# Optimization experiments

Hardware: AMD Instinct MI355X
Metric: run time of the kernel (lower is better)

Reference implementation:

```python
import jax, jax.numpy as jnp
import numpy as np

N_EMBD = 2048
N_HEAD = 16
N_INNER = 8192
EPS = 1e-5


def _wn_weight(v, g):
    # torch weight_norm with dim=1 on weight [out, in]:
    # w[:, j] = g[j] * v[:, j] / ||v[:, j]||_2
    norm = jnp.sqrt(jnp.sum(v * v, axis=0))  # [in]
    return v * (g / norm)[None, :]


def _layer_norm(x, gamma, beta):
    mu = jnp.mean(x, axis=-1, keepdims=True)
    var = jnp.mean(jnp.square(x - mu), axis=-1, keepdims=True)
    return (x - mu) * jax.lax.rsqrt(var + EPS) * gamma + beta


def setup_inputs() -> dict:
    key = jax.random.key(0)
    ks = jax.random.split(key, 12)
    E, I, H = N_EMBD, N_INNER, N_HEAD
    s = lambda n: 1.0 / np.sqrt(n)
    return {
        "hidden_states": jax.random.normal(ks[0], (2, 2048, E), jnp.float32),
        "ln1_g": jnp.ones((E,), jnp.float32),
        "ln1_b": jnp.zeros((E,), jnp.float32),
        "w_qkv": jax.random.normal(ks[1], (3 * E, E), jnp.float32) * s(E),
        "b_qkv": jnp.zeros((3 * E,), jnp.float32),
        "attn_proj_v": jax.random.normal(ks[2], (E, E), jnp.float32) * s(E),
        "attn_proj_g": jnp.abs(jax.random.normal(ks[3], (E,), jnp.float32)) + 0.5,
        "attn_proj_b": jnp.zeros((E,), jnp.float32),
        "emotion_bias": jax.random.normal(ks[4], (H,), jnp.float32) * 0.1,
        "ln2_g": jnp.ones((E,), jnp.float32),
        "ln2_b": jnp.zeros((E,), jnp.float32),
        "w_fc": jax.random.normal(ks[5], (I, E), jnp.float32) * s(E),
        "b_fc": jnp.zeros((I,), jnp.float32),
        "mlp_proj_v": jax.random.normal(ks[6], (E, I), jnp.float32) * s(I),
        "mlp_proj_g": jnp.abs(jax.random.normal(ks[7], (I,), jnp.float32)) + 0.5,
        "mlp_proj_b": jnp.zeros((E,), jnp.float32),
    }


def reference(hidden_states, ln1_g, ln1_b, w_qkv, b_qkv, attn_proj_v, attn_proj_g,
              attn_proj_b, emotion_bias, ln2_g, ln2_b, w_fc, b_fc,
              mlp_proj_v, mlp_proj_g, mlp_proj_b):
    B, S, E = hidden_states.shape
    H = N_HEAD
    D = E // H

    # --- attention sub-block ---
    residual = hidden_states
    x = _layer_norm(hidden_states, ln1_g, ln1_b)
    qkv = x @ w_qkv.T + b_qkv                       # [B,S,3E]
    q, k, v = jnp.split(qkv, 3, axis=-1)
    q = q.reshape(B, S, H, D).transpose(0, 2, 1, 3)  # [B,H,S,D]
    k = k.reshape(B, S, H, D).transpose(0, 2, 1, 3)
    v = v.reshape(B, S, H, D).transpose(0, 2, 1, 3)

    scores = jnp.einsum("bhqd,bhkd->bhqk", q, k) / jnp.sqrt(jnp.float32(D))
    scores = scores + emotion_bias[None, :, None, None]
    probs = jax.nn.softmax(scores, axis=-1)
    attn = jnp.einsum("bhqk,bhkd->bhqd", probs, v)   # [B,H,S,D]
    attn = attn.transpose(0, 2, 1, 3).reshape(B, S, E)
    w_proj = _wn_weight(attn_proj_v, attn_proj_g)
    attn = attn @ w_proj.T + attn_proj_b

    hidden = attn + residual

    # --- MLP sub-block ---
    residual = hidden
    x = _layer_norm(hidden, ln2_g, ln2_b)
    h = jax.nn.gelu(x @ w_fc.T + b_fc, approximate=False)
    w_proj2 = _wn_weight(mlp_proj_v, mlp_proj_g)
    h = h @ w_proj2.T + mlp_proj_b
    return residual + h
```

## Files before the change

### kernel.cpp

```cpp
#include <hip/hip_runtime.h>
#include <hip/hip_bf16.h>

#define DEVI __device__ __forceinline__

typedef __attribute__((ext_vector_type(8))) __bf16 bf16x8;
typedef __attribute__((ext_vector_type(4))) float f32x4;
typedef __attribute__((ext_vector_type(4))) unsigned short u16x4;
typedef __attribute__((ext_vector_type(8))) unsigned short u16x8;

DEVI unsigned short f2bf(float f) {
  unsigned int u = __float_as_uint(f);
  u += 0x7FFFu + ((u >> 16) & 1u);
  return (unsigned short)(u >> 16);
}

#define GLD16(g, l) __builtin_amdgcn_global_load_lds(                      \
    (const __attribute__((address_space(1))) void*)(g),                    \
    (__attribute__((address_space(3))) void*)(l), 16, 0, 0)


__global__ __launch_bounds__(256) void cast_k(const float* __restrict__ in,
                                              unsigned short* __restrict__ out,
                                              int n4) {
  for (int i = blockIdx.x * 256 + threadIdx.x; i < n4; i += gridDim.x * 256) {
    f32x4 v = ((const f32x4*)in)[i];
    u16x4 o;
    o.x = f2bf(v.x); o.y = f2bf(v.y); o.z = f2bf(v.z); o.w = f2bf(v.w);
    ((u16x4*)out)[i] = o;
  }
}

__global__ __launch_bounds__(256) void colnorm1_k(const float* __restrict__ v,
                                                  float* __restrict__ part,
                                                  int cols) {
  const int tid = threadIdx.x;
  const int g = tid & 127;
  const int s = tid >> 7;
  const int c0 = blockIdx.x * 512;
  const int r0 = blockIdx.y * 64 + s * 32;
  const float* base = v + (size_t)r0 * cols + c0 + g * 4;
  f32x4 acc = {};
#pragma unroll 4
  for (int i = 0; i < 32; ++i) {
    f32x4 x = *(const f32x4*)(base + (size_t)i * cols);
    acc.x += x.x * x.x; acc.y += x.y * x.y;
    acc.z += x.z * x.z; acc.w += x.w * x.w;
  }
  __shared__ f32x4 red[256];
  red[tid] = acc;
  __syncthreads();
  if (s == 0) {
    f32x4 a = red[tid], b = red[tid + 128];
    f32x4 o;
    o.x = a.x + b.x; o.y = a.y + b.y; o.z = a.z + b.z; o.w = a.w + b.w;
    *(f32x4*)(part + (size_t)blockIdx.y * cols + c0 + g * 4) = o;
  }
}

__global__ __launch_bounds__(256) void colnorm2_k(const float* __restrict__ part,
                                                  const float* __restrict__ g,
                                                  float* __restrict__ s,
                                                  int cols, int nrc) {
  const int c = blockIdx.x * 256 + threadIdx.x;
  float acc = 0.f;
  for (int i = 0; i < nrc; ++i) acc += part[(size_t)i * cols + c];
  s[c] = g[c] * rsqrtf(acc);
}

__global__ __launch_bounds__(256) void scale_cast_k(const float* __restrict__ in,
                                                    const float* __restrict__ s,
                                                    unsigned short* __restrict__ out,
                                                    int cols, int n4) {
  const int cmask4 = (cols >> 2) - 1;
  for (int i = blockIdx.x * 256 + threadIdx.x; i < n4; i += gridDim.x * 256) {
    f32x4 v = ((const f32x4*)in)[i];
    f32x4 sv = ((const f32x4*)s)[i & cmask4];
    u16x4 o;
    o.x = f2bf(v.x * sv.x); o.y = f2bf(v.y * sv.y);
    o.z = f2bf(v.z * sv.z); o.w = f2bf(v.w * sv.w);
    ((u16x4*)out)[i] = o;
  }
}

__global__ __launch_bounds__(256) void ln_k(const float* __restrict__ x,
                                            const float* __restrict__ g,
                                            const float* __restrict__ b,
                                            unsigned short* __restrict__ out) {
  const int tid = threadIdx.x, lane = tid & 63, wid = tid >> 6;
  const int row = blockIdx.x;
  const float* xr = x + (size_t)row * 2048;
  f32x4 a0 = ((const f32x4*)xr)[tid];
  f32x4 a1 = ((const f32x4*)xr)[tid + 256];
  float s = a0.x + a0.y + a0.z + a0.w + a1.x + a1.y + a1.z + a1.w;
  float ss = a0.x * a0.x + a0.y * a0.y + a0.z * a0.z + a0.w * a0.w +
             a1.x * a1.x + a1.y * a1.y + a1.z * a1.z + a1.w * a1.w;
#pragma unroll
  for (int m = 1; m < 64; m <<= 1) {
    s += __shfl_xor(s, m);
    ss += __shfl_xor(ss, m);
  }
  __shared__ float red[8];
  if (lane == 0) { red[wid] = s; red[4 + wid] = ss; }
  __syncthreads();
  s = red[0] + red[1] + red[2] + red[3];
  ss = red[4] + red[5] + red[6] + red[7];
  const float mu = s * (1.f / 2048.f);
  const float var = ss * (1.f / 2048.f) - mu * mu;
  const float rs = rsqrtf(var + 1e-5f);
  f32x4 g0 = ((const f32x4*)g)[tid], g1 = ((const f32x4*)g)[tid + 256];
  f32x4 b0 = ((const f32x4*)b)[tid], b1 = ((const f32x4*)b)[tid + 256];
  u16x4 o0, o1;
  o0.x = f2bf((a0.x - mu) * rs * g0.x + b0.x);
  o0.y = f2bf((a0.y - mu) * rs * g0.y + b0.y);
  o0.z = f2bf((a0.z - mu) * rs * g0.z + b0.z);
  o0.w = f2bf((a0.w - mu) * rs * g0.w + b0.w);
  o1.x = f2bf((a1.x - mu) * rs * g1.x + b1.x);
  o1.y = f2bf((a1.y - mu) * rs * g1.y + b1.y);
  o1.z = f2bf((a1.z - mu) * rs * g1.z + b1.z);
  o1.w = f2bf((a1.w - mu) * rs * g1.w + b1.w);
  unsigned short* orow = out + (size_t)row * 2048;
  *(u16x4*)(orow + 4 * tid) = o0;
  *(u16x4*)(orow + 1024 + 4 * tid) = o1;
}

__global__ __launch_bounds__(256) void vtrans_k(const unsigned short* __restrict__ v,
                                                unsigned short* __restrict__ vt) {
  __shared__ unsigned short t[64][134];
  const int tid = threadIdx.x;
  const int bh = blockIdx.x >> 5, st = blockIdx.x & 31;
  const unsigned short* vb = v + ((size_t)bh << 18) + ((size_t)(st << 6) << 7);
#pragma unroll
  for (int i = 0; i < 4; ++i) {
    int f = tid + (i << 8);
    int row = f >> 4, c8 = f & 15;
    u16x8 x = *(const u16x8*)(vb + row * 128 + c8 * 8);
#pragma unroll
    for (int j = 0; j < 4; ++j) {
      unsigned int pk = ((unsigned int)x[2 * j + 1] << 16) | x[2 * j];
      *(unsigned int*)&t[row][c8 * 8 + 2 * j] = pk;
    }
  }
  __syncthreads();
  const int lane = tid & 63, wid = tid >> 6;
  unsigned short* ob = vt + ((size_t)bh << 18) + (st << 6);
#pragma unroll
  for (int j = 0; j < 32; ++j) {
    int d = (wid << 5) + j;
    ob[((size_t)d << 11) + lane] = t[lane][d];
  }
}

__global__ __launch_bounds__(256) void g4red_k(const float* __restrict__ p0,
                                               const float* __restrict__ p1,
                                               const float* __restrict__ bias,
                                               const float* __restrict__ res,
                                               float* __restrict__ out, int n4) {
  for (int i = blockIdx.x * 256 + threadIdx.x; i < n4; i += gridDim.x * 256) {
    f32x4 a = ((const f32x4*)p0)[i];
    f32x4 b = ((const f32x4*)p1)[i];
    f32x4 r = ((const f32x4*)res)[i];
    f32x4 bb = ((const f32x4*)bias)[i & 511];
    f32x4 o;
    o.x = a.x + b.x + r.x + bb.x;
    o.y = a.y + b.y + r.y + bb.y;
    o.z = a.z + b.z + r.z + bb.z;
    o.w = a.w + b.w + r.w + bb.w;
    ((f32x4*)out)[i] = o;
  }
}

struct GemmP {
  const unsigned short* A;
  const unsigned short* B;
  const float* bias;
  const float* res;
  float* outF;
  unsigned short* outH;
  unsigned short* q;
  unsigned short* k;
  unsigned short* vt;
  int M, N, K;
};

template <int EPI>
DEVI void gemm128_body(const GemmP& p, int m0, int n0, int k0, int nk) {
  const int tid = threadIdx.x, lane = tid & 63, wid = tid >> 6;
  const int K = p.K;
  const int wr = wid >> 1, wc = wid & 1;

  __shared__ __align__(16) unsigned short sA[2][4096];
  __shared__ __align__(16) unsigned short sB[2][4096];

  const int c0 = tid, c1 = tid + 256;
  const unsigned short* gA0 = p.A + (size_t)(m0 + (c0 >> 2)) * K + k0 + ((c0 & 3) << 3);
  const unsigned short* gA1 = p.A + (size_t)(m0 + (c1 >> 2)) * K + k0 + ((c1 & 3) << 3);
  const unsigned short* gB0 = p.B + (size_t)(n0 + (c0 >> 2)) * K + k0 + ((c0 & 3) << 3);
  const unsigned short* gB1 = p.B + (size_t)(n0 + (c1 >> 2)) * K + k0 + ((c1 & 3) << 3);
  const int l0 = wid << 9, l1 = (wid << 9) + 2048;

  f32x4 acc[4][4] = {};
  const int arow = (wr << 6) + (lane & 15);
  const int brow = (wc << 6) + (lane & 15);
  const int koff = (lane >> 4) << 3;

#define STAGE128(bufi, t) do { int ko = (t) << 5;       \
    GLD16(gA0 + ko, &sA[bufi][l0]);                     \
    GLD16(gA1 + ko, &sA[bufi][l1]);                     \
    GLD16(gB0 + ko, &sB[bufi][l0]);                     \
    GLD16(gB1 + ko, &sB[bufi][l1]); } while (0)

  STAGE128(0, 0);
  __syncthreads();
  int cur = 0;
  for (int t = 0; t < nk; ++t) {
    if (t + 1 < nk) STAGE128(cur ^ 1, t + 1);
    bf16x8 af[4], bfr[4];
#pragma unroll
    for (int i = 0; i < 4; ++i)
      af[i] = *(const bf16x8*)&sA[cur][(arow + (i << 4)) * 32 + koff];
#pragma unroll
    for (int i = 0; i < 4; ++i)
      bfr[i] = *(const bf16x8*)&sB[cur][(brow + (i << 4)) * 32 + koff];
#pragma unroll
    for (int i = 0; i < 4; ++i)
#pragma unroll
      for (int j = 0; j < 4; ++j)
        acc[i][j] = __builtin_amdgcn_mfma_f32_16x16x32_bf16(af[i], bfr[j], acc[i][j], 0, 0, 0);
    __syncthreads();
    cur ^= 1;
  }
#undef STAGE128

  const int rbase = m0 + (wr << 6) + ((lane >> 4) << 2);
  const int cbase = n0 + (wc << 6) + (lane & 15);
#pragma unroll
  for (int mi = 0; mi < 4; ++mi) {
#pragma unroll
    for (int ni = 0; ni < 4; ++ni) {
      const int col = cbase + (ni << 4);
#pragma unroll
      for (int r = 0; r < 4; ++r) {
        const int row = rbase + (mi << 4) + r;
        if constexpr (EPI == 0) {
          float v = acc[mi][ni][r] + p.bias[col];
          const int gsel = col >> 11, e = col & 2047;
          const int h = e >> 7, d = e & 127;
          const int b2 = row >> 11, sidx = row & 2047;
          const size_t off = ((size_t)(b2 * 16 + h) << 18) + ((size_t)sidx << 7) + d;
          unsigned short hv = f2bf(v);
          if (gsel == 0)      p.q[off] = hv;
          else if (gsel == 1) p.k[off] = hv;
          else                p.vt[off] = hv;
        } else if constexpr (EPI == 1) {
          const size_t o = (size_t)row * p.N + col;
          p.outF[o] = acc[mi][ni][r] + p.bias[col] + p.res[o];
        } else {
          p.outF[(size_t)row * p.N + col] = acc[mi][ni][r];
        }
      }
    }
  }
}

__global__ __launch_bounds__(256) void g1_qkv128(GemmP p) {
  const int x = blockIdx.x & 7, i = blockIdx.x >> 3;
  const int bm = i & 31;
  const int bn = x * 6 + (i >> 5);
  gemm128_body<0>(p, bm << 7, bn << 7, 0, p.K >> 5);
}
__global__ __launch_bounds__(256) void g2_proj128(GemmP p) {
  const int x = blockIdx.x & 7, i = blockIdx.x >> 3;
  const int bm = (x >> 1) * 8 + (i >> 3);
  const int bn = (x & 1) * 8 + (i & 7);
  gemm128_body<1>(p, bm << 7, bn << 7, 0, p.K >> 5);
}
__global__ __launch_bounds__(256) void g4_splitk(GemmP p) {
  const int x = blockIdx.x & 7, i = blockIdx.x >> 3;
  const int ks = i & 1, j = i >> 1;
  const int bm = (x >> 1) * 8 + (j >> 3);
  const int bn = (x & 1) * 8 + (j & 7);
  GemmP q = p;
  q.outF = p.outF + (size_t)ks * 4096 * 2048;
  gemm128_body<4>(q, bm << 7, bn << 7, ks << 12, 128);
}

DEVI void setup256(const GemmP& p, int m0, int n0,
                   const unsigned short*& gsA0, const unsigned short*& gsA1,
                   const unsigned short*& gsB0, const unsigned short*& gsB1) {
  const int tid = threadIdx.x;
  int r_[2], c_[2];
#pragma unroll
  for (int j = 0; j < 2; ++j) {
    int d = tid * 16 + j * 8192;
    int w = (d & 1023) ^ (((d >> 9) & 1) << 5);
    r_[j] = ((d >> 10) << 4) + (w >> 6);
    c_[j] = (w & 63) >> 1;
  }
  gsA0 = p.A + (size_t)(m0 + r_[0]) * p.K + c_[0];
  gsA1 = p.A + (size_t)(m0 + r_[1]) * p.K + c_[1];
  gsB0 = p.B + (size_t)(n0 + r_[0]) * p.K + c_[0];
  gsB1 = p.B + (size_t)(n0 + r_[1]) * p.K + c_[1];
}

DEVI void epi256g(const GemmP& p, f32x4 (&acc)[8][4], int m0, int n0) {
  const int lane = threadIdx.x & 63, wid = threadIdx.x >> 6;
  const int wr = wid >> 2, wc = wid & 3;
  const int lr = lane & 15, lk = lane >> 4;
  const int rbase = m0 + wr * 128 + (lk << 2);
  const int cbase = n0 + wc * 64 + lr;
#pragma unroll
  for (int m = 0; m < 8; ++m) {
#pragma unroll
    for (int n = 0; n < 4; ++n) {
      const int col = cbase + (n << 4);
      const float bb = p.bias[col];
#pragma unroll
      for (int r = 0; r < 4; ++r) {
        const int row = rbase + (m << 4) + r;
        float v = acc[m][n][r] + bb;
        float y = 0.7978845608028654f * (v + 0.044715f * v * v * v);
        float u = __expf(2.f * y);
        float gl = (y > 40.f) ? v : v * (u / (u + 1.f));
        p.outH[(size_t)row * p.N + col] = f2bf(gl);
      }
    }
  }
}

DEVI void gemm8p_body(const GemmP& p, unsigned short* lds_raw, int m0, int n0) {
  const int tid = threadIdx.x, lane = tid & 63, wid = tid >> 6;
  const int wr = wid >> 2, wc = wid & 3;
  const int lr = lane & 15, lk = lane >> 4;
  const int fb = (lr * 64 + lk * 16) ^ ((lr & 8) << 2);

  const unsigned short *gsA0, *gsA1, *gsB0, *gsB1;
  setup256(p, m0, n0, gsA0, gsA1, gsB0, gsB1);

#define STAGE_A8(b, kt) do { unsigned short* _d = lds_raw + ((b) << 14);       \
    GLD16(gsA0 + ((size_t)(kt) << 5), _d + (tid << 3));                        \
    GLD16(gsA1 + ((size_t)(kt) << 5), _d + 4096 + (tid << 3)); } while (0)
#define STAGE_B8(b, kt) do { unsigned short* _d = lds_raw + ((b) << 14) + 8192;\
    GLD16(gsB0 + ((size_t)(kt) << 5), _d + (tid << 3));                        \
    GLD16(gsB1 + ((size_t)(kt) << 5), _d + 4096 + (tid << 3)); } while (0)

  f32x4 acc[8][4] = {};
  const int NK = p.K >> 5;

  STAGE_A8(0, 0); STAGE_B8(0, 0);
  STAGE_A8(1, 1); STAGE_B8(1, 1);
  STAGE_A8(2, 2); STAGE_B8(2, 2);
  asm volatile("s_waitcnt vmcnt(8)" ::: "memory");
  __builtin_amdgcn_s_barrier();

  for (int t = 0; t < NK; ++t) {
    const int bi = t & 3;
    const char* tA = (const char*)(lds_raw + (bi << 14));
    const char* tB = (const char*)(lds_raw + (bi << 14) + 8192);
    bf16x8 a_[4], b_[4];
#pragma unroll
    for (int n = 0; n < 4; ++n)
      b_[n] = *(const bf16x8*)(tB + (((wc << 2) + n) << 10) + fb);
#pragma unroll
    for (int m = 0; m < 4; ++m)
      a_[m] = *(const bf16x8*)(tA + (((wr << 3) + m) << 10) + fb);
    if (t + 3 < NK) STAGE_A8((t + 3) & 3, t + 3);
    __builtin_amdgcn_s_barrier();
    asm volatile("s_waitcnt lgkmcnt(0)" ::: "memory");
    __builtin_amdgcn_sched_barrier(0);
    __builtin_amdgcn_s_setprio(1);
#pragma unroll
    for (int m = 0; m < 4; ++m)
#pragma unroll
      for (int n = 0; n < 4; ++n)
        acc[m][n] = __builtin_amdgcn_mfma_f32_16x16x32_bf16(a_[m], b_[n], acc[m][n], 0, 0, 0);
    __builtin_amdgcn_s_setprio(0);
    __builtin_amdgcn_s_barrier();
#pragma unroll
    for (int m = 0; m < 4; ++m)
      a_[m] = *(const bf16x8*)(tA + (((wr << 3) + 4 + m) << 10) + fb);
    if (t + 3 < NK) STAGE_B8((t + 3) & 3, t + 3);
    if (t + 3 < NK)      asm volatile("s_waitcnt vmcnt(8)" ::: "memory");
    else if (t + 2 < NK) asm volatile("s_waitcnt vmcnt(4)" ::: "memory");
    else if (t + 1 < NK) asm volatile("s_waitcnt vmcnt(0)" ::: "memory");
    __builtin_amdgcn_s_barrier();
    asm volatile("s_waitcnt lgkmcnt(0)" ::: "memory");
    __builtin_amdgcn_sched_barrier(0);
    __builtin_amdgcn_s_setprio(1);
#pragma unroll
    for (int m = 0; m < 4; ++m)
#pragma unroll
      for (int n = 0; n < 4; ++n)
        acc[4 + m][n] = __builtin_amdgcn_mfma_f32_16x16x32_bf16(a_[m], b_[n], acc[4 + m][n], 0, 0, 0);
    __builtin_amdgcn_s_setprio(0);
    __builtin_amdgcn_s_barrier();
  }
#undef STAGE_A8
#undef STAGE_B8
  epi256g(p, acc, m0, n0);
}

DEVI void gemm2p_body(const GemmP& p, unsigned short* lds_raw, int m0, int n0) {
  const int tid = threadIdx.x, lane = tid & 63, wid = tid >> 6;
  const int wr = wid >> 2, wc = wid & 3;
  const int lr = lane & 15, lk = lane >> 4;
  const int fb = (lr * 64 + lk * 16) ^ ((lr & 8) << 2);

  const unsigned short *gsA0, *gsA1, *gsB0, *gsB1;
  setup256(p, m0, n0, gsA0, gsA1, gsB0, gsB1);

#define STG2(b, kt) do { unsigned short* _d = lds_raw + ((b) << 14);     \
    GLD16(gsA0 + ((size_t)(kt) << 5), _d + (tid << 3));                  \
    GLD16(gsA1 + ((size_t)(kt) << 5), _d + 4096 + (tid << 3));           \
    GLD16(gsB0 + ((size_t)(kt) << 5), _d + 8192 + (tid << 3));           \
    GLD16(gsB1 + ((size_t)(kt) << 5), _d + 12288 + (tid << 3)); } while (0)

  f32x4 acc[8][4] = {};
  const int NK = p.K >> 5;
  STG2(0, 0);
  __syncthreads();
  int cur = 0;
  for (int t = 0; t < NK; ++t) {
    if (t + 1 < NK) STG2(cur ^ 1, t + 1);
    const char* tA = (const char*)(lds_raw + (cur << 14));
    const char* tB = tA + 16384;
    bf16x8 a_[8], b_[4];
#pragma unroll
    for (int n = 0; n < 4; ++n)
      b_[n] = *(const bf16x8*)(tB + (((wc << 2) + n) << 10) + fb);
#pragma unroll
    for (int m = 0; m < 8; ++m)
      a_[m] = *(const bf16x8*)(tA + (((wr << 3) + m) << 10) + fb);
#pragma unroll
    for (int m = 0; m < 8; ++m)
#pragma unroll
      for (int n = 0; n < 4; ++n)
        acc[m][n] = __builtin_amdgcn_mfma_f32_16x16x32_bf16(a_[m], b_[n], acc[m][n], 0, 0, 0);
    __syncthreads();
    cur ^= 1;
  }
#undef STG2
  epi256g(p, acc, m0, n0);
}

__global__ __launch_bounds__(512, 2) void g3a_fc8p(GemmP p) {
  extern __shared__ unsigned short lds_raw[];
  const int x = blockIdx.x & 7, i = blockIdx.x >> 3;
  const int bm = (x >> 2) * 4 + (i >> 3);
  const int bn = (x & 3) * 8 + (i & 7);
  gemm8p_body(p, lds_raw, bm << 8, bn << 8);
}
__global__ __launch_bounds__(512, 2) void g3b_fc2p(GemmP p) {
  extern __shared__ unsigned short lds_raw[];
  const int x = blockIdx.x & 7, i = blockIdx.x >> 3;
  const int bm = (x >> 2) * 4 + (i >> 3);
  const int bn = (x & 3) * 8 + (i & 7);
  gemm2p_body(p, lds_raw, 2048 + (bm << 8), bn << 8);
}

__global__ __launch_bounds__(256) void attn_k(const unsigned short* __restrict__ Q,
                                              const unsigned short* __restrict__ Kg,
                                              const unsigned short* __restrict__ Vt,
                                              unsigned short* __restrict__ O) {
  const int tid = threadIdx.x, lane = tid & 63, wid = tid >> 6;
  const int bid = blockIdx.x;
  const int pos = bid >> 3;
  const int bh = (bid & 7) * 4 + (pos >> 5);
  const int qt = pos & 31;
  const int q0 = qt * 64 + wid * 16;
  const int b = bh >> 4, h = bh & 15;

  __shared__ __align__(16) unsigned short sK[64 * 128];
  __shared__ __align__(16) unsigned short sV[128 * 64];
  __shared__ __align__(16) unsigned short sP[4][16 * 72];

  const unsigned short* Qb = Q + ((size_t)bh << 18);
  const unsigned short* Kb = Kg + ((size_t)bh << 18);
  const unsigned short* Vb = Vt + ((size_t)bh << 18);

  bf16x8 qf[4];
  {
    const unsigned short* qp = Qb + (size_t)(q0 + (lane & 15)) * 128 + ((lane >> 4) << 3);
#pragma unroll
    for (int kk = 0; kk < 4; ++kk) qf[kk] = *(const bf16x8*)(qp + kk * 32);
  }

  int koffs[4], voffs[4];
#pragma unroll
  for (int i = 0; i < 4; ++i) {
    const int c = tid + (i << 8);
    const int kv = c >> 4, jj = c & 15;
    const int js = (jj & 8) | ((jj ^ kv) & 7);
    koffs[i] = kv * 128 + (js << 3);
    const int d = c >> 3, j2 = c & 7;
    const int js2 = j2 ^ (d & 7);
    voffs[i] = d * 2048 + (js2 << 3);
  }
  u16x8 kreg[4], vreg[4];
  auto PREF = [&](int kt) {
    const int kv0 = kt << 6;
#pragma unroll
    for (int i = 0; i < 4; ++i) {
      kreg[i] = *(const u16x8*)(Kb + kv0 * 128 + koffs[i]);
      vreg[i] = *(const u16x8*)(Vb + kv0 + voffs[i]);
    }
  };

  f32x4 oacc[8] = {};
  float mrun = -3e38f, lrun = 0.f;
  PREF(0);

  for (int kt = 0; kt < 32; ++kt) {
#pragma unroll
    for (int i = 0; i < 4; ++i) {
      const int c8 = (tid + (i << 8)) << 3;
      *(u16x8*)&sK[c8] = kreg[i];
      *(u16x8*)&sV[c8] = vreg[i];
    }
    __syncthreads();
    if (kt + 1 < 32) PREF(kt + 1);

    f32x4 sc[4] = {};
    __builtin_amdgcn_s_setprio(1);
#pragma unroll
    for (int ti = 0; ti < 4; ++ti) {
#pragma unroll
      for (int kk = 0; kk < 4; ++kk) {
        const int row = (ti << 4) + (lane & 15);
        int bo = (row << 8) + (kk << 6) + ((lane >> 4) << 4);
        bo ^= (row & 7) << 4;
        bf16x8 kf = *(const bf16x8*)((const char*)sK + bo);
        sc[ti] = __builtin_amdgcn_mfma_f32_16x16x32_bf16(kf, qf[kk], sc[ti], 0, 0, 0);
      }
    }
    __builtin_amdgcn_s_setprio(0);

    float pv[16];
    float mx = -3e38f;
#pragma unroll
    for (int ti = 0; ti < 4; ++ti)
#pragma unroll
      for (int r = 0; r < 4; ++r) {
        float x = sc[ti][r] * 0.08838834764831845f;
        pv[(ti << 2) + r] = x;
        mx = fmaxf(mx, x);
      }
    mx = fmaxf(mx, __shfl_xor(mx, 16));
    mx = fmaxf(mx, __shfl_xor(mx, 32));

    float corr = 1.f;
    if (!__all(mx - mrun <= 8.f)) {
      const float mnew = fmaxf(mrun, mx);
      corr = __expf(mrun - mnew);
      mrun = mnew;
      float fr[4];
#pragma unroll
      for (int r = 0; r < 4; ++r) fr[r] = __shfl(corr, ((lane >> 4) << 2) + r);
#pragma unroll
      for (int di = 0; di < 8; ++di)
#pragma unroll
        for (int r = 0; r < 4; ++r) oacc[di][r] *= fr[r];
    }
    float psum = 0.f;
#pragma unroll
    for (int i2 = 0; i2 < 16; ++i2) {
      float e = __expf(pv[i2] - mrun);
      pv[i2] = e;
      psum += e;
    }
    psum += __shfl_xor(psum, 16);
    psum += __shfl_xor(psum, 32);
    lrun = lrun * corr + psum;

    unsigned short* prow = &sP[wid][(lane & 15) * 72];
#pragma unroll
    for (int ti = 0; ti < 4; ++ti) {
      u16x4 w4;
      w4.x = f2bf(pv[(ti << 2) + 0]);
      w4.y = f2bf(pv[(ti << 2) + 1]);
      w4.z = f2bf(pv[(ti << 2) + 2]);
      w4.w = f2bf(pv[(ti << 2) + 3]);
      *(u16x4*)&prow[(ti << 4) + ((lane >> 4) << 2)] = w4;
    }

    __builtin_amdgcn_s_setprio(1);
#pragma unroll
    for (int di = 0; di < 8; ++di) {
#pragma unroll
      for (int ks = 0; ks < 2; ++ks) {
        bf16x8 pf = *(const bf16x8*)((const char*)&sP[wid][0] +
                                     (lane & 15) * 144 + (ks << 6) + ((lane >> 4) << 4));
        const int dr = (di << 4) + (lane & 15);
        int bo = (dr << 7) + (ks << 6) + ((lane >> 4) << 4);
        bo ^= (dr & 7) << 4;
        bf16x8 vf = *(const bf16x8*)((const char*)sV + bo);
        oacc[di] = __builtin_amdgcn_mfma_f32_16x16x32_bf16(pf, vf, oacc[di], 0, 0, 0);
      }
    }
    __builtin_amdgcn_s_setprio(0);
    __syncthreads();
  }

  float il[4];
#pragma unroll
  for (int r = 0; r < 4; ++r) il[r] = 1.f / __shfl(lrun, ((lane >> 4) << 2) + r);
  const size_t obase = ((size_t)(b * 2048 + q0)) * 2048 + h * 128;
#pragma unroll
  for (int di = 0; di < 8; ++di)
#pragma unroll
    for (int r = 0; r < 4; ++r) {
      const size_t o = obase + (size_t)(((lane >> 4) << 2) + r) * 2048 + (di << 4) + (lane & 15);
      O[o] = f2bf(oacc[di][r] * il[r]);
    }
}


extern "C" void kernel_launch(void* const* d_in, const int* in_sizes, int n_in,
                              void* d_out, int out_size, void* d_ws, size_t ws_size,
                              hipStream_t stream) {
  (void)in_sizes; (void)n_in; (void)out_size; (void)ws_size;
  const float* hidden = (const float*)d_in[0];
  const float* ln1_g = (const float*)d_in[1];
  const float* ln1_b = (const float*)d_in[2];
  const float* w_qkv = (const float*)d_in[3];
  const float* b_qkv = (const float*)d_in[4];
  const float* apv = (const float*)d_in[5];
  const float* apg = (const float*)d_in[6];
  const float* apb = (const float*)d_in[7];
  const float* ln2_g = (const float*)d_in[9];
  const float* ln2_b = (const float*)d_in[10];
  const float* w_fc = (const float*)d_in[11];
  const float* b_fc = (const float*)d_in[12];
  const float* mpv = (const float*)d_in[13];
  const float* mpg = (const float*)d_in[14];
  const float* mpb = (const float*)d_in[15];

  char* w = (char*)d_ws;
  const size_t MBs = 1ull << 20;
  float* hidden2 = (float*)(w + 0);
  unsigned short* vbuf = (unsigned short*)(w + 32 * MBs);
  unsigned short* vtbuf = (unsigned short*)(w + 48 * MBs);
  unsigned short* hbuf = (unsigned short*)(w + 32 * MBs);
  unsigned short* qbuf = (unsigned short*)(w + 96 * MBs);
  unsigned short* kbuf = (unsigned short*)(w + 112 * MBs);
  unsigned short* xln = (unsigned short*)(w + 128 * MBs);
  unsigned short* xln2 = (unsigned short*)(w + 144 * MBs);
  unsigned short* wqkv_bf = (unsigned short*)(w + 160 * MBs);
  unsigned short* w2_bf = (unsigned short*)(w + 160 * MBs);
  unsigned short* wproj_bf = (unsigned short*)(w + 192 * MBs);
  float* s_attn = (float*)(w + 200 * MBs);
  float* s_mlp = (float*)(w + 200 * MBs + 32768);
  float* part_attn = (float*)(w + 201 * MBs);
  float* part_mlp = (float*)(w + 202 * MBs);
  unsigned short* wfc_bf = qbuf;
  float* part0 = (float*)(w + 96 * MBs);
  float* part1 = (float*)(w + 128 * MBs);

  hipFuncSetAttribute((const void*)g3a_fc8p, hipFuncAttributeMaxDynamicSharedMemorySize, 131072);
  hipFuncSetAttribute((const void*)g3b_fc2p, hipFuncAttributeMaxDynamicSharedMemorySize, 65536);

  cast_k<<<2048, 256, 0, stream>>>(w_qkv, wqkv_bf, (6144 * 2048) / 4);
  colnorm1_k<<<dim3(4, 32), 256, 0, stream>>>(apv, part_attn, 2048);
  colnorm2_k<<<8, 256, 0, stream>>>(part_attn, apg, s_attn, 2048, 32);
  scale_cast_k<<<2048, 256, 0, stream>>>(apv, s_attn, wproj_bf, 2048, (2048 * 2048) / 4);
  colnorm1_k<<<dim3(16, 32), 256, 0, stream>>>(mpv, part_mlp, 8192);
  colnorm2_k<<<32, 256, 0, stream>>>(part_mlp, mpg, s_mlp, 8192, 32);

  ln_k<<<4096, 256, 0, stream>>>(hidden, ln1_g, ln1_b, xln);

  GemmP p1 = {xln, wqkv_bf, b_qkv, nullptr, nullptr, nullptr,
              qbuf, kbuf, vbuf, 4096, 6144, 2048};
  g1_qkv128<<<1536, 256, 0, stream>>>(p1);

  vtrans_k<<<1024, 256, 0, stream>>>(vbuf, vtbuf);

  attn_k<<<1024, 256, 0, stream>>>(qbuf, kbuf, vtbuf, xln);

  cast_k<<<2048, 256, 0, stream>>>(w_fc, wfc_bf, (8192 * 2048) / 4);
  scale_cast_k<<<4096, 256, 0, stream>>>(mpv, s_mlp, w2_bf, 8192, (2048 * 8192) / 4);

  GemmP p2 = {xln, wproj_bf, apb, hidden, hidden2, nullptr,
              nullptr, nullptr, nullptr, 4096, 2048, 2048};
  g2_proj128<<<512, 256, 0, stream>>>(p2);

  ln_k<<<4096, 256, 0, stream>>>(hidden2, ln2_g, ln2_b, xln2);

  GemmP p3 = {xln2, wfc_bf, b_fc, nullptr, nullptr, hbuf,
              nullptr, nullptr, nullptr, 4096, 8192, 2048};
  g3a_fc8p<<<256, 512, 131072, stream>>>(p3);
  g3b_fc2p<<<256, 512, 65536, stream>>>(p3);

  GemmP p4 = {hbuf, w2_bf, mpb, nullptr, part0, nullptr,
              nullptr, nullptr, nullptr, 4096, 2048, 8192};
  g4_splitk<<<1024, 256, 0, stream>>>(p4);
  g4red_k<<<2048, 256, 0, stream>>>(part0, part1, mpb, hidden2, (float*)d_out,
                                    (4096 * 2048) / 4);
}
```

Measured before the change: 887.7 us.

## Write QKV row-major and use 4-way bf16 split-K partials for MLP projection

The QKV GEMM epilogue now writes one contiguous bf16 [tokens, 6144] buffer instead of scattered per-head Q/K/V stores, and the attention and V-transpose kernels index that strided layout directly. The final MLP projection moves from a 2-way split-K with fp32 partials to a 4-way split with bf16 partials, so the reduction kernel sums four half-width arrays. The aim is coalesced epilogue stores, less partial traffic and more blocks for the last GEMM. The cost is bf16 rounding of the partial sums, which lowers accuracy, and strided K/Q loads in attention.

```diff
diff --git a/kernel.cpp b/kernel.cpp
--- a/kernel.cpp
+++ b/kernel.cpp
@@ -12,6 +12,9 @@
   unsigned int u = __float_as_uint(f);
   u += 0x7FFFu + ((u >> 16) & 1u);
   return (unsigned short)(u >> 16);
+}
+DEVI float bf2f(unsigned short u) {
+  return __uint_as_float(((unsigned int)u) << 16);
 }
 
 #define GLD16(g, l) __builtin_amdgcn_global_load_lds(                      \
@@ -123,17 +126,18 @@
   *(u16x4*)(orow + 1024 + 4 * tid) = o1;
 }
 
-__global__ __launch_bounds__(256) void vtrans_k(const unsigned short* __restrict__ v,
+__global__ __launch_bounds__(256) void vtrans_k(const unsigned short* __restrict__ qkv,
                                                 unsigned short* __restrict__ vt) {
   __shared__ unsigned short t[64][134];
   const int tid = threadIdx.x;
   const int bh = blockIdx.x >> 5, st = blockIdx.x & 31;
-  const unsigned short* vb = v + ((size_t)bh << 18) + ((size_t)(st << 6) << 7);
+  const int b = bh >> 4, h = bh & 15;
+  const unsigned short* vb = qkv + (size_t)(b * 2048 + st * 64) * 6144 + 4096 + h * 128;
 #pragma unroll
   for (int i = 0; i < 4; ++i) {
     int f = tid + (i << 8);
     int row = f >> 4, c8 = f & 15;
-    u16x8 x = *(const u16x8*)(vb + row * 128 + c8 * 8);
+    u16x8 x = *(const u16x8*)(vb + (size_t)row * 6144 + c8 * 8);
 #pragma unroll
     for (int j = 0; j < 4; ++j) {
       unsigned int pk = ((unsigned int)x[2 * j + 1] << 16) | x[2 * j];
@@ -150,21 +154,23 @@
   }
 }
 
-__global__ __launch_bounds__(256) void g4red_k(const float* __restrict__ p0,
-                                               const float* __restrict__ p1,
+__global__ __launch_bounds__(256) void g4red_k(const unsigned short* __restrict__ parts,
                                                const float* __restrict__ bias,
                                                const float* __restrict__ res,
                                                float* __restrict__ out, int n4) {
+  const size_t PS = (size_t)4096 * 2048;
   for (int i = blockIdx.x * 256 + threadIdx.x; i < n4; i += gridDim.x * 256) {
-    f32x4 a = ((const f32x4*)p0)[i];
-    f32x4 b = ((const f32x4*)p1)[i];
+    u16x4 a = ((const u16x4*)(parts))[i];
+    u16x4 b = ((const u16x4*)(parts + PS))[i];
+    u16x4 c = ((const u16x4*)(parts + 2 * PS))[i];
+    u16x4 d = ((const u16x4*)(parts + 3 * PS))[i];
     f32x4 r = ((const f32x4*)res)[i];
     f32x4 bb = ((const f32x4*)bias)[i & 511];
     f32x4 o;
-    o.x = a.x + b.x + r.x + bb.x;
-    o.y = a.y + b.y + r.y + bb.y;
-    o.z = a.z + b.z + r.z + bb.z;
-    o.w = a.w + b.w + r.w + bb.w;
+    o.x = bf2f(a.x) + bf2f(b.x) + bf2f(c.x) + bf2f(d.x) + r.x + bb.x;
+    o.y = bf2f(a.y) + bf2f(b.y) + bf2f(c.y) + bf2f(d.y) + r.y + bb.y;
+    o.z = bf2f(a.z) + bf2f(b.z) + bf2f(c.z) + bf2f(d.z) + r.z + bb.z;
+    o.w = bf2f(a.w) + bf2f(b.w) + bf2f(c.w) + bf2f(d.w) + r.w + bb.w;
     ((f32x4*)out)[i] = o;
   }
 }
@@ -176,9 +182,6 @@
   const float* res;
   float* outF;
   unsigned short* outH;
-  unsigned short* q;
-  unsigned short* k;
-  unsigned short* vt;
   int M, N, K;
 };
 
@@ -242,20 +245,12 @@
       for (int r = 0; r < 4; ++r) {
         const int row = rbase + (mi << 4) + r;
         if constexpr (EPI == 0) {
-          float v = acc[mi][ni][r] + p.bias[col];
-          const int gsel = col >> 11, e = col & 2047;
-          const int h = e >> 7, d = e & 127;
-          const int b2 = row >> 11, sidx = row & 2047;
-          const size_t off = ((size_t)(b2 * 16 + h) << 18) + ((size_t)sidx << 7) + d;
-          unsigned short hv = f2bf(v);
-          if (gsel == 0)      p.q[off] = hv;
-          else if (gsel == 1) p.k[off] = hv;
-          else                p.vt[off] = hv;
+          p.outH[(size_t)row * p.N + col] = f2bf(acc[mi][ni][r] + p.bias[col]);
         } else if constexpr (EPI == 1) {
           const size_t o = (size_t)row * p.N + col;
           p.outF[o] = acc[mi][ni][r] + p.bias[col] + p.res[o];
         } else {
-          p.outF[(size_t)row * p.N + col] = acc[mi][ni][r];
+          p.outH[(size_t)row * p.N + col] = f2bf(acc[mi][ni][r]);
         }
       }
     }
@@ -276,12 +271,12 @@
 }
 __global__ __launch_bounds__(256) void g4_splitk(GemmP p) {
   const int x = blockIdx.x & 7, i = blockIdx.x >> 3;
-  const int ks = i & 1, j = i >> 1;
+  const int ks = i & 3, j = i >> 2;
   const int bm = (x >> 1) * 8 + (j >> 3);
   const int bn = (x & 1) * 8 + (j & 7);
   GemmP q = p;
-  q.outF = p.outF + (size_t)ks * 4096 * 2048;
-  gemm128_body<4>(q, bm << 7, bn << 7, ks << 12, 128);
+  q.outH = p.outH + (size_t)ks * 4096 * 2048;
+  gemm128_body<5>(q, bm << 7, bn << 7, ks << 11, 64);
 }
 
 DEVI void setup256(const GemmP& p, int m0, int n0,
@@ -457,8 +452,7 @@
   gemm2p_body(p, lds_raw, 2048 + (bm << 8), bn << 8);
 }
 
-__global__ __launch_bounds__(256) void attn_k(const unsigned short* __restrict__ Q,
-                                              const unsigned short* __restrict__ Kg,
+__global__ __launch_bounds__(256) void attn_k(const unsigned short* __restrict__ qkv,
                                               const unsigned short* __restrict__ Vt,
                                               unsigned short* __restrict__ O) {
   const int tid = threadIdx.x, lane = tid & 63, wid = tid >> 6;
@@ -473,13 +467,13 @@
   __shared__ __align__(16) unsigned short sV[128 * 64];
   __shared__ __align__(16) unsigned short sP[4][16 * 72];
 
-  const unsigned short* Qb = Q + ((size_t)bh << 18);
-  const unsigned short* Kb = Kg + ((size_t)bh << 18);
+  const unsigned short* Qb = qkv + (size_t)(b * 2048) * 6144 + h * 128;
+  const unsigned short* Kb = qkv + (size_t)(b * 2048) * 6144 + 2048 + h * 128;
   const unsigned short* Vb = Vt + ((size_t)bh << 18);
 
   bf16x8 qf[4];
   {
-    const unsigned short* qp = Qb + (size_t)(q0 + (lane & 15)) * 128 + ((lane >> 4) << 3);
+    const unsigned short* qp = Qb + (size_t)(q0 + (lane & 15)) * 6144 + ((lane >> 4) << 3);
 #pragma unroll
     for (int kk = 0; kk < 4; ++kk) qf[kk] = *(const bf16x8*)(qp + kk * 32);
   }
@@ -490,7 +484,7 @@
     const int c = tid + (i << 8);
     const int kv = c >> 4, jj = c & 15;
     const int js = (jj & 8) | ((jj ^ kv) & 7);
-    koffs[i] = kv * 128 + (js << 3);
+    koffs[i] = kv * 6144 + (js << 3);
     const int d = c >> 3, j2 = c & 7;
     const int js2 = j2 ^ (d & 7);
     voffs[i] = d * 2048 + (js2 << 3);
@@ -498,9 +492,10 @@
   u16x8 kreg[4], vreg[4];
   auto PREF = [&](int kt) {
     const int kv0 = kt << 6;
+    const unsigned short* kb = Kb + (size_t)kv0 * 6144;
 #pragma unroll
     for (int i = 0; i < 4; ++i) {
-      kreg[i] = *(const u16x8*)(Kb + kv0 * 128 + koffs[i]);
+      kreg[i] = *(const u16x8*)(kb + koffs[i]);
       vreg[i] = *(const u16x8*)(Vb + kv0 + voffs[i]);
     }
   };
@@ -636,14 +631,15 @@
 
   char* w = (char*)d_ws;
   const size_t MBs = 1ull << 20;
+  unsigned short* xln = (unsigned short*)(w + 0);
   float* hidden2 = (float*)(w + 0);
-  unsigned short* vbuf = (unsigned short*)(w + 32 * MBs);
-  unsigned short* vtbuf = (unsigned short*)(w + 48 * MBs);
+  unsigned short* vtbuf = (unsigned short*)(w + 32 * MBs);
   unsigned short* hbuf = (unsigned short*)(w + 32 * MBs);
-  unsigned short* qbuf = (unsigned short*)(w + 96 * MBs);
-  unsigned short* kbuf = (unsigned short*)(w + 112 * MBs);
-  unsigned short* xln = (unsigned short*)(w + 128 * MBs);
-  unsigned short* xln2 = (unsigned short*)(w + 144 * MBs);
+  unsigned short* qkv = (unsigned short*)(w + 96 * MBs);
+  unsigned short* wfc_bf = (unsigned short*)(w + 96 * MBs);
+  unsigned short* xln2 = (unsigned short*)(w + 128 * MBs);
+  unsigned short* attn_out = (unsigned short*)(w + 144 * MBs);
+  unsigned short* partH = (unsigned short*)(w + 96 * MBs);
   unsigned short* wqkv_bf = (unsigned short*)(w + 160 * MBs);
   unsigned short* w2_bf = (unsigned short*)(w + 160 * MBs);
   unsigned short* wproj_bf = (unsigned short*)(w + 192 * MBs);
@@ -651,9 +647,6 @@
   float* s_mlp = (float*)(w + 200 * MBs + 32768);
   float* part_attn = (float*)(w + 201 * MBs);
   float* part_mlp = (float*)(w + 202 * MBs);
-  unsigned short* wfc_bf = qbuf;
-  float* part0 = (float*)(w + 96 * MBs);
-  float* part1 = (float*)(w + 128 * MBs);
 
   hipFuncSetAttribute((const void*)g3a_fc8p, hipFuncAttributeMaxDynamicSharedMemorySize, 131072);
   hipFuncSetAttribute((const void*)g3b_fc2p, hipFuncAttributeMaxDynamicSharedMemorySize, 65536);
@@ -667,31 +660,27 @@
 
   ln_k<<<4096, 256, 0, stream>>>(hidden, ln1_g, ln1_b, xln);
 
-  GemmP p1 = {xln, wqkv_bf, b_qkv, nullptr, nullptr, nullptr,
-              qbuf, kbuf, vbuf, 4096, 6144, 2048};
+  GemmP p1 = {xln, wqkv_bf, b_qkv, nullptr, nullptr, qkv, 4096, 6144, 2048};
   g1_qkv128<<<1536, 256, 0, stream>>>(p1);
 
-  vtrans_k<<<1024, 256, 0, stream>>>(vbuf, vtbuf);
-
-  attn_k<<<1024, 256, 0, stream>>>(qbuf, kbuf, vtbuf, xln);
+  vtrans_k<<<1024, 256, 0, stream>>>(qkv, vtbuf);
+
+  attn_k<<<1024, 256, 0, stream>>>(qkv, vtbuf, attn_out);
 
   cast_k<<<2048, 256, 0, stream>>>(w_fc, wfc_bf, (8192 * 2048) / 4);
   scale_cast_k<<<4096, 256, 0, stream>>>(mpv, s_mlp, w2_bf, 8192, (2048 * 8192) / 4);
 
-  GemmP p2 = {xln, wproj_bf, apb, hidden, hidden2, nullptr,
-              nullptr, nullptr, nullptr, 4096, 2048, 2048};
+  GemmP p2 = {attn_out, wproj_bf, apb, hidden, hidden2, nullptr, 4096, 2048, 2048};
   g2_proj128<<<512, 256, 0, stream>>>(p2);
 
   ln_k<<<4096, 256, 0, stream>>>(hidden2, ln2_g, ln2_b, xln2);
 
-  GemmP p3 = {xln2, wfc_bf, b_fc, nullptr, nullptr, hbuf,
-              nullptr, nullptr, nullptr, 4096, 8192, 2048};
+  GemmP p3 = {xln2, wfc_bf, b_fc, nullptr, nullptr, hbuf, 4096, 8192, 2048};
   g3a_fc8p<<<256, 512, 131072, stream>>>(p3);
   g3b_fc2p<<<256, 512, 65536, stream>>>(p3);
 
-  GemmP p4 = {hbuf, w2_bf, mpb, nullptr, part0, nullptr,
-              nullptr, nullptr, nullptr, 4096, 2048, 8192};
-  g4_splitk<<<1024, 256, 0, stream>>>(p4);
-  g4red_k<<<2048, 256, 0, stream>>>(part0, part1, mpb, hidden2, (float*)d_out,
+  GemmP p4 = {hbuf, w2_bf, mpb, nullptr, nullptr, partH, 4096, 2048, 8192};
+  g4_splitk<<<2048, 256, 0, stream>>>(p4);
+  g4red_k<<<2048, 256, 0, stream>>>(partH, mpb, hidden2, (float*)d_out,
                                     (4096 * 2048) / 4);
 }
```

Measured after the change: 898.1 us. Within noise of the previous version (+1.2%).
